# Kernel optimization log

Measured on AMD Instinct MI355X. Metric: run time of the kernel, lower is better.

Reference implementation:

```python
import jax, jax.numpy as jnp
import numpy as np

B, L, D = 1, 4096, 1024
N_AR, N_DIFF, D_HEAD = 8, 8, 64
H = N_AR + N_DIFF
ROPE_BASE = 10000.0


def rotate_half(x):
    x1, x2 = jnp.split(x, 2, axis=-1)
    return jnp.concatenate([-x2, x1], axis=-1)


def rope_cos_sin(seq_len, d_head):
    inv_freq = 1.0 / (ROPE_BASE ** (jnp.arange(0, d_head, 2, dtype=jnp.float32) / d_head))
    t = jnp.arange(seq_len, dtype=jnp.float32)
    freqs = t[:, None] * inv_freq[None, :]          # [L, d_head//2]
    emb = jnp.concatenate([freqs, freqs], axis=-1)  # [L, d_head]
    return jnp.cos(emb), jnp.sin(emb)


def setup_inputs() -> dict:
    key = jax.random.key(0)
    ks = jax.random.split(key, 5)
    return {
        "hidden_states": jax.random.normal(ks[0], (B, L, D), dtype=jnp.float32),
        "Wq": jax.random.normal(ks[1], (D, H * D_HEAD), dtype=jnp.float32) * 0.02,
        "Wk": jax.random.normal(ks[2], (D, H * D_HEAD), dtype=jnp.float32) * 0.02,
        "Wv": jax.random.normal(ks[3], (D, H * D_HEAD), dtype=jnp.float32) * 0.02,
        "Wo": jax.random.normal(ks[4], (H * D_HEAD, D), dtype=jnp.float32) * 0.02,
    }


def _attend(q, k, v, mask):
    # q,k,v: [B, h, L, d]; mask: [L, L] additive
    scale = D_HEAD ** -0.5
    scores = jnp.einsum("bhqd,bhkd->bhqk", q, k) * scale + mask
    attn = jax.nn.softmax(scores.astype(jnp.float32), axis=-1).astype(q.dtype)
    return jnp.einsum("bhqk,bhkd->bhqd", attn, v)


def reference(hidden_states, Wq, Wk, Wv, Wo):
    b, l, _ = hidden_states.shape

    def heads(x, W):
        return (x @ W).reshape(b, l, H, D_HEAD).transpose(0, 2, 1, 3)  # [B,H,L,d]

    q = heads(hidden_states, Wq)
    k = heads(hidden_states, Wk)
    v = heads(hidden_states, Wv)

    cos, sin = rope_cos_sin(l, D_HEAD)  # [L, d]
    q = q * cos + rotate_half(q) * sin
    k = k * cos + rotate_half(k) * sin

    neg_inf = jnp.finfo(jnp.float32).min
    causal = jnp.where(jnp.tril(jnp.ones((l, l), dtype=bool)), 0.0, -jnp.inf).astype(jnp.float32)

    out_ar = _attend(q[:, :N_AR], k[:, :N_AR], v[:, :N_AR], causal)
    out_diff = _attend(q[:, N_AR:], k[:, N_AR:], v[:, N_AR:], jnp.zeros((l, l), jnp.float32))

    out = jnp.concatenate([out_ar, out_diff], axis=1)          # [B,H,L,d]
    out = out.transpose(0, 2, 1, 3).reshape(b, l, H * D_HEAD)  # [B,L,H*d]
    return out @ Wo
```

## Files before the change

kernel.cpp:

```cpp
#include <hip/hip_runtime.h>

#define LSEQ 4096
#define DMODEL 1024
#define HTOT 16
#define NAR 8
#define DHEAD 64
#define QKVS 3072

typedef unsigned short u16;
typedef unsigned int u32;
typedef __attribute__((ext_vector_type(8))) short bf16x8;
typedef __attribute__((ext_vector_type(4))) short bf16x4;
typedef __attribute__((ext_vector_type(4))) float f32x4;
typedef __attribute__((ext_vector_type(4))) unsigned int u32x4;

typedef __attribute__((address_space(1))) void gvoid;
typedef __attribute__((address_space(3))) void lvoid;

__device__ __forceinline__ void cp16(const void* g, void* l) {
    __builtin_amdgcn_global_load_lds((gvoid*)(void*)g, (lvoid*)l, 16, 0, 0);
}

__device__ __forceinline__ u16 f2bf(float f) {
    u32 x = __float_as_uint(f);
    return (u16)((x + 0x7fffu + ((x >> 16) & 1u)) >> 16);
}
__device__ __forceinline__ u32 packtr(float lo, float hi) {
    return __builtin_amdgcn_perm(__float_as_uint(hi), __float_as_uint(lo), 0x07060302u);
}

__global__ __launch_bounds__(256) void xcast(const float* __restrict__ X, u16* __restrict__ Xb)
{
    const size_t i = (size_t)(blockIdx.x * 256 + threadIdx.x) * 8;
    float4 a0 = *(const float4*)(X + i);
    float4 a1 = *(const float4*)(X + i + 4);
    uint4 pk;
    pk.x = packtr(a0.x, a0.y); pk.y = packtr(a0.z, a0.w);
    pk.z = packtr(a1.x, a1.y); pk.w = packtr(a1.z, a1.w);
    *(uint4*)(Xb + i) = pk;
}

__global__ __launch_bounds__(256) void transp_cvt3(
    const float* __restrict__ Wq, const float* __restrict__ Wk,
    const float* __restrict__ Wv, u16* __restrict__ D)
{
    __shared__ u16 T[64][72];
    const float* S = (blockIdx.z == 0) ? Wq : ((blockIdx.z == 1) ? Wk : Wv);
    u16* Dz = D + (size_t)blockIdx.z * 1024 * 1024;
    const int tid = threadIdx.x;
    const int bx = blockIdx.x, by = blockIdx.y;
#pragma unroll
    for (int i = 0; i < 4; ++i) {
        int id = tid + i * 256;
        int fr = id >> 4, fc = id & 15;
        float4 v = *(const float4*)(S + (size_t)(by * 64 + fr) * 1024 + bx * 64 + fc * 4);
        T[fc * 4 + 0][fr] = f2bf(v.x);
        T[fc * 4 + 1][fr] = f2bf(v.y);
        T[fc * 4 + 2][fr] = f2bf(v.z);
        T[fc * 4 + 3][fr] = f2bf(v.w);
    }
    __syncthreads();
#pragma unroll
    for (int i = 0; i < 2; ++i) {
        int id = tid + i * 256;
        int c = id >> 3, g = id & 7;
        *(uint4*)(Dz + (size_t)(bx * 64 + c) * 1024 + by * 64 + g * 8) = *(const uint4*)&T[c][g * 8];
    }
}

__global__ __launch_bounds__(256) void transp_cvt(
    const float* __restrict__ S, u16* __restrict__ D)
{
    __shared__ u16 T[64][72];
    const int tid = threadIdx.x;
    const int bx = blockIdx.x, by = blockIdx.y;
#pragma unroll
    for (int i = 0; i < 4; ++i) {
        int id = tid + i * 256;
        int fr = id >> 4, fc = id & 15;
        float4 v = *(const float4*)(S + (size_t)(by * 64 + fr) * 1024 + bx * 64 + fc * 4);
        T[fc * 4 + 0][fr] = f2bf(v.x);
        T[fc * 4 + 1][fr] = f2bf(v.y);
        T[fc * 4 + 2][fr] = f2bf(v.z);
        T[fc * 4 + 3][fr] = f2bf(v.w);
    }
    __syncthreads();
#pragma unroll
    for (int i = 0; i < 2; ++i) {
        int id = tid + i * 256;
        int c = id >> 3, g = id & 7;
        *(uint4*)(D + (size_t)(bx * 64 + c) * 1024 + by * 64 + g * 8) = *(const uint4*)&T[c][g * 8];
    }
}

__global__ __launch_bounds__(256) void gemm_qkv(
    const u16* __restrict__ A, const u16* __restrict__ Bt, u16* __restrict__ C)
{
    __shared__ u16 As[2][128][32];
    __shared__ u16 Bs[2][128][32];
    const int tid = threadIdx.x;
    const int lane = tid & 63, w = tid >> 6;
    const int col = lane & 15, quad = lane >> 4;
    const int bm = blockIdx.y << 7, bn = blockIdx.x << 7;
    const int wm = (w & 1) << 6, wn = (w >> 1) << 6;
    const int sr = lane >> 2, sc = (lane & 3) << 3;
    const f32x4 zero = {0.f, 0.f, 0.f, 0.f};
    f32x4 acc[4][4];
#pragma unroll
    for (int i = 0; i < 4; ++i)
#pragma unroll
        for (int j = 0; j < 4; ++j) acc[i][j] = zero;

#pragma unroll
    for (int i = 0; i < 2; ++i) {
        const int r0 = w * 32 + i * 16;
        cp16(A  + (size_t)(bm + r0 + sr) * 1024 + sc, &As[0][r0][0]);
        cp16(Bt + (size_t)(bn + r0 + sr) * 1024 + sc, &Bs[0][r0][0]);
    }

    for (int kc = 0; kc < 32; ++kc) {
        const int cur = kc & 1, nxt = cur ^ 1;
        __syncthreads();
        if (kc + 1 < 32) {
            const int k1 = (kc + 1) * 32;
#pragma unroll
            for (int i = 0; i < 2; ++i) {
                const int r0 = w * 32 + i * 16;
                cp16(A  + (size_t)(bm + r0 + sr) * 1024 + k1 + sc, &As[nxt][r0][0]);
                cp16(Bt + (size_t)(bn + r0 + sr) * 1024 + k1 + sc, &Bs[nxt][r0][0]);
            }
        }
        bf16x8 af[4], bfr[4];
#pragma unroll
        for (int i = 0; i < 4; ++i) af[i] = *(const bf16x8*)&As[cur][wm + i * 16 + col][quad * 8];
#pragma unroll
        for (int j = 0; j < 4; ++j) bfr[j] = *(const bf16x8*)&Bs[cur][wn + j * 16 + col][quad * 8];
#pragma unroll
        for (int i = 0; i < 4; ++i)
#pragma unroll
            for (int j = 0; j < 4; ++j)
                acc[i][j] = __builtin_amdgcn_mfma_f32_16x16x32_bf16(af[i], bfr[j], acc[i][j], 0, 0, 0);
    }

    if (blockIdx.x < 16) {
        const float scale = (blockIdx.x < 8) ? 0.18033688011112042f : 1.0f;
        const float inv0 = __expf((float)col * -0.2878231366242557f);
        const float inv1 = __expf((float)(16 + col) * -0.2878231366242557f);
#pragma unroll
        for (int i = 0; i < 4; ++i)
#pragma unroll
            for (int r = 0; r < 4; ++r) {
                const float t = (float)(bm + wm + i * 16 + quad * 4 + r);
                float s0, c0, s1, c1;
                __sincosf(t * inv0, &s0, &c0);
                __sincosf(t * inv1, &s1, &c1);
                float a0 = acc[i][0][r], b0 = acc[i][2][r];
                acc[i][0][r] = (a0 * c0 - b0 * s0) * scale;
                acc[i][2][r] = (b0 * c0 + a0 * s0) * scale;
                float a1 = acc[i][1][r], b1 = acc[i][3][r];
                acc[i][1][r] = (a1 * c1 - b1 * s1) * scale;
                acc[i][3][r] = (b1 * c1 + a1 * s1) * scale;
            }
    }
#pragma unroll
    for (int i = 0; i < 4; ++i)
#pragma unroll
        for (int j = 0; j < 4; ++j)
#pragma unroll
            for (int r = 0; r < 4; ++r)
                C[(size_t)(bm + wm + i * 16 + quad * 4 + r) * QKVS + bn + wn + j * 16 + col] =
                    f2bf(acc[i][j][r]);
}

__global__ __launch_bounds__(256) void gemm_out(
    const u16* __restrict__ A, const u16* __restrict__ Bt, float* __restrict__ C)
{
    __shared__ u16 As[2][128][32];
    __shared__ u16 Bs[2][64][32];
    const int tid = threadIdx.x;
    const int lane = tid & 63, w = tid >> 6;
    const int col = lane & 15, quad = lane >> 4;
    const int bm = blockIdx.y << 7, bn = blockIdx.x << 6;
    const int wm = (w & 1) << 6, wn = (w >> 1) << 5;
    const int sr = lane >> 2, sc = (lane & 3) << 3;
    const f32x4 zero = {0.f, 0.f, 0.f, 0.f};
    f32x4 acc[4][2];
#pragma unroll
    for (int i = 0; i < 4; ++i)
#pragma unroll
        for (int j = 0; j < 2; ++j) acc[i][j] = zero;

    {
#pragma unroll
        for (int i = 0; i < 2; ++i) {
            const int r0 = w * 32 + i * 16;
            cp16(A + (size_t)(bm + r0 + sr) * 1024 + sc, &As[0][r0][0]);
        }
        cp16(Bt + (size_t)(bn + w * 16 + sr) * 1024 + sc, &Bs[0][w * 16][0]);
    }

    for (int kc = 0; kc < 32; ++kc) {
        const int cur = kc & 1, nxt = cur ^ 1;
        __syncthreads();
        if (kc + 1 < 32) {
            const int k1 = (kc + 1) * 32;
#pragma unroll
            for (int i = 0; i < 2; ++i) {
                const int r0 = w * 32 + i * 16;
                cp16(A + (size_t)(bm + r0 + sr) * 1024 + k1 + sc, &As[nxt][r0][0]);
            }
            cp16(Bt + (size_t)(bn + w * 16 + sr) * 1024 + k1 + sc, &Bs[nxt][w * 16][0]);
        }
        bf16x8 af[4], bfr[2];
#pragma unroll
        for (int i = 0; i < 4; ++i) af[i] = *(const bf16x8*)&As[cur][wm + i * 16 + col][quad * 8];
#pragma unroll
        for (int j = 0; j < 2; ++j) bfr[j] = *(const bf16x8*)&Bs[cur][wn + j * 16 + col][quad * 8];
#pragma unroll
        for (int i = 0; i < 4; ++i)
#pragma unroll
            for (int j = 0; j < 2; ++j)
                acc[i][j] = __builtin_amdgcn_mfma_f32_16x16x32_bf16(af[i], bfr[j], acc[i][j], 0, 0, 0);
    }
#pragma unroll
    for (int i = 0; i < 4; ++i)
#pragma unroll
        for (int j = 0; j < 2; ++j)
#pragma unroll
            for (int r = 0; r < 4; ++r)
                C[(size_t)(bm + wm + i * 16 + quad * 4 + r) * 1024 + bn + wn + j * 16 + col] =
                    acc[i][j][r];
}

__global__ __launch_bounds__(256) void attn_mfma(
    const u16* __restrict__ QKV, u16* __restrict__ AO)
{
    __shared__ u16 Ks[2][128][64];
    __shared__ u16 Vt[64][136];
    const int bid = blockIdx.x;
    int h, qt;
    if (bid < 256) { h = 8 + (bid & 7); qt = bid >> 3; }
    else { int i = bid - 256; h = i & 7; qt = 31 - (i >> 3); }
    const bool causal = (h < NAR);
    const int tid = threadIdx.x;
    const int w = tid >> 6, lane = tid & 63;
    const int col = lane & 15, quad = lane >> 4;
    const int qb = qt * 128;
    const int qr0 = qb + w * 32 + col;
    const int qr1 = qr0 + 16;
    const int cva = ((lane >> 1) & 3) * 32 + (lane >> 3) * 4 + (lane & 1) * 2;

    bf16x8 qf[2][2];
#pragma unroll
    for (int s = 0; s < 2; ++s)
#pragma unroll
        for (int ks = 0; ks < 2; ++ks)
            qf[s][ks] = *(const bf16x8*)(QKV + (size_t)(qr0 + s * 16) * QKVS +
                                         h * DHEAD + ks * 32 + quad * 8);

    bf16x8 ones8;
#pragma unroll
    for (int i = 0; i < 8; ++i) ones8[i] = (short)0x3F80;

    const f32x4 zero = {0.f, 0.f, 0.f, 0.f};
    f32x4 O[2][5];
#pragma unroll
    for (int s = 0; s < 2; ++s)
#pragma unroll
        for (int nd = 0; nd < 5; ++nd) O[s][nd] = zero;

    const int nch = causal ? (qt + 1) : (LSEQ / 128);
    const int krow = lane >> 3;
    const int kcb = (lane & 7) ^ krow;
    const u16* kbase = QKV + (size_t)krow * QKVS + 1024 + h * DHEAD + kcb * 8;
    const u16* vbase = QKV + (size_t)(lane * 2) * QKVS + 2048 + h * DHEAD + w * 16;

    u32x4 vA0, vA1, vB0, vB1;
    bf16x8 pf8[2][4];

#define VT_WRITE()                                                                                 \
    _Pragma("unroll")                                                                              \
    for (int j = 0; j < 4; ++j) {                                                                  \
        *(u32*)&Vt[w * 16 + 2 * j][cva]         = __builtin_amdgcn_perm(vB0[j], vA0[j], 0x05040100u); \
        *(u32*)&Vt[w * 16 + 2 * j + 1][cva]     = __builtin_amdgcn_perm(vB0[j], vA0[j], 0x07060302u); \
        *(u32*)&Vt[w * 16 + 8 + 2 * j][cva]     = __builtin_amdgcn_perm(vB1[j], vA1[j], 0x05040100u); \
        *(u32*)&Vt[w * 16 + 8 + 2 * j + 1][cva] = __builtin_amdgcn_perm(vB1[j], vA1[j], 0x07060302u); \
    }

#define PV_STEP()                                                                                  \
    {                                                                                              \
        __builtin_amdgcn_s_setprio(1);                                                             \
        _Pragma("unroll")                                                                          \
        for (int tp = 0; tp < 4; ++tp) {                                                           \
            bf16x8 vv[4];                                                                          \
            _Pragma("unroll")                                                                      \
            for (int nd = 0; nd < 4; ++nd)                                                         \
                vv[nd] = *(const bf16x8*)&Vt[nd * 16 + col][quad * 32 + tp * 8];                   \
            _Pragma("unroll")                                                                      \
            for (int nd = 0; nd < 4; ++nd) {                                                       \
                O[0][nd] = __builtin_amdgcn_mfma_f32_16x16x32_bf16(vv[nd], pf8[0][tp], O[0][nd], 0, 0, 0); \
                O[1][nd] = __builtin_amdgcn_mfma_f32_16x16x32_bf16(vv[nd], pf8[1][tp], O[1][nd], 0, 0, 0); \
            }                                                                                      \
            O[0][4] = __builtin_amdgcn_mfma_f32_16x16x32_bf16(ones8, pf8[0][tp], O[0][4], 0, 0, 0); \
            O[1][4] = __builtin_amdgcn_mfma_f32_16x16x32_bf16(ones8, pf8[1][tp], O[1][4], 0, 0, 0); \
        }                                                                                          \
        __builtin_amdgcn_s_setprio(0);                                                             \
    }

#define S_STEP(KBUF, CH)                                                                           \
    {                                                                                              \
        const bool mask = causal && ((CH) == qt);                                                  \
        _Pragma("unroll")                                                                          \
        for (int hf = 0; hf < 2; ++hf) {                                                           \
            f32x4 st[2][4];                                                                        \
            _Pragma("unroll")                                                                      \
            for (int s = 0; s < 2; ++s)                                                            \
                _Pragma("unroll")                                                                  \
                for (int jj = 0; jj < 4; ++jj) st[s][jj] = zero;                                   \
            __builtin_amdgcn_s_setprio(1);                                                         \
            _Pragma("unroll")                                                                      \
            for (int ks = 0; ks < 2; ++ks)                                                         \
                _Pragma("unroll")                                                                  \
                for (int jj = 0; jj < 4; ++jj) {                                                   \
                    bf16x8 kf = *(const bf16x8*)&Ks[KBUF][(hf * 4 + jj) * 16 + col]                \
                                                         [((ks * 4 + quad) ^ (col & 7)) * 8];      \
                    st[0][jj] = __builtin_amdgcn_mfma_f32_16x16x32_bf16(kf, qf[0][ks], st[0][jj], 0, 0, 0); \
                    st[1][jj] = __builtin_amdgcn_mfma_f32_16x16x32_bf16(kf, qf[1][ks], st[1][jj], 0, 0, 0); \
                }                                                                                  \
            __builtin_amdgcn_s_setprio(0);                                                         \
            if (mask) {                                                                            \
                _Pragma("unroll")                                                                  \
                for (int jj = 0; jj < 4; ++jj) {                                                   \
                    const int kk = (CH) * 128 + (hf * 4 + jj) * 16 + quad * 4;                     \
                    _Pragma("unroll")                                                              \
                    for (int r = 0; r < 4; ++r) {                                                  \
                        if (kk + r > qr0) st[0][jj][r] = -1e30f;                                   \
                        if (kk + r > qr1) st[1][jj][r] = -1e30f;                                   \
                    }                                                                              \
                }                                                                                  \
            }                                                                                      \
            _Pragma("unroll")                                                                      \
            for (int s = 0; s < 2; ++s)                                                            \
                _Pragma("unroll")                                                                  \
                for (int jj = 0; jj < 4; ++jj) {                                                   \
                    u32 plo = packtr(__builtin_amdgcn_exp2f(st[s][jj][0]),                         \
                                     __builtin_amdgcn_exp2f(st[s][jj][1]));                        \
                    u32 phi = packtr(__builtin_amdgcn_exp2f(st[s][jj][2]),                         \
                                     __builtin_amdgcn_exp2f(st[s][jj][3]));                        \
                    u32* p = (u32*)&pf8[s][0] + (hf * 4 + jj) * 2;                                 \
                    p[0] = plo; p[1] = phi;                                                        \
                }                                                                                  \
        }                                                                                          \
    }

#pragma unroll
    for (int i = 0; i < 4; ++i)
        cp16(kbase + (size_t)((i * 4 + w) * 8) * QKVS, &Ks[0][(i * 4 + w) * 8][0]);
    vA0 = *(u32x4*)(vbase);
    vA1 = *(u32x4*)(vbase + 8);
    vB0 = *(u32x4*)(vbase + QKVS);
    vB1 = *(u32x4*)(vbase + QKVS + 8);
    __syncthreads();
    VT_WRITE();
    if (nch > 1) {
#pragma unroll
        for (int i = 0; i < 4; ++i)
            cp16(kbase + (size_t)(128 + (i * 4 + w) * 8) * QKVS, &Ks[1][(i * 4 + w) * 8][0]);
    }
    S_STEP(0, 0);

    for (int ch = 1; ch < nch; ++ch) {
        const int cur = ch & 1;
        __syncthreads();
        if (ch + 1 < nch) {
            const size_t c1 = (size_t)(ch + 1) * 128;
#pragma unroll
            for (int i = 0; i < 4; ++i)
                cp16(kbase + (c1 + (i * 4 + w) * 8) * QKVS, &Ks[cur ^ 1][(i * 4 + w) * 8][0]);
        }
        {
            const u16* vp = vbase + (size_t)ch * 128 * QKVS;
            vA0 = *(u32x4*)(vp);
            vA1 = *(u32x4*)(vp + 8);
            vB0 = *(u32x4*)(vp + QKVS);
            vB1 = *(u32x4*)(vp + QKVS + 8);
        }
        PV_STEP();
        S_STEP(cur, ch);
        __syncthreads();
        VT_WRITE();
    }

    __syncthreads();
    PV_STEP();

#pragma unroll
    for (int s = 0; s < 2; ++s) {
        const float inv = 1.f / O[s][4][0];
        const int qrow = qr0 + s * 16;
#pragma unroll
        for (int nd = 0; nd < 4; ++nd) {
            ushort4 ov;
            ov.x = f2bf(O[s][nd][0] * inv);
            ov.y = f2bf(O[s][nd][1] * inv);
            ov.z = f2bf(O[s][nd][2] * inv);
            ov.w = f2bf(O[s][nd][3] * inv);
            *(ushort4*)(AO + (size_t)qrow * 1024 + h * DHEAD + nd * 16 + quad * 4) = ov;
        }
    }
#undef VT_WRITE
#undef PV_STEP
#undef S_STEP
}

extern "C" void kernel_launch(void* const* d_in, const int* in_sizes, int n_in,
                              void* d_out, int out_size, void* d_ws, size_t ws_size,
                              hipStream_t stream)
{
    const float* X  = (const float*)d_in[0];
    const float* Wq = (const float*)d_in[1];
    const float* Wk = (const float*)d_in[2];
    const float* Wv = (const float*)d_in[3];
    const float* Wo = (const float*)d_in[4];
    float* out = (float*)d_out;

    u16* Wt  = (u16*)d_ws;
    u16* AOb = (u16*)d_ws;
    u16* QKV = (u16*)d_ws + (size_t)4 * 1024 * 1024;
    u16* Wot = QKV;
    u16* Xb  = (u16*)out;

    xcast<<<2048, 256, 0, stream>>>(X, Xb);
    transp_cvt3<<<dim3(16, 16, 3), 256, 0, stream>>>(Wq, Wk, Wv, Wt);
    gemm_qkv<<<dim3(24, 32), 256, 0, stream>>>(Xb, Wt, QKV);
    attn_mfma<<<512, 256, 0, stream>>>(QKV, AOb);
    transp_cvt<<<dim3(16, 16), 256, 0, stream>>>(Wo, Wot);
    gemm_out<<<dim3(16, 32), 256, 0, stream>>>(AOb, Wot, out);
}
```

Measured before the change: 241.8 us.

## Split non-causal attention tiles across two blocks and merge partials

Most non-causal (diffusion) head tiles are split into two key-range halves computed by separate blocks. Each half writes unnormalized fp32 partial outputs and row sums to scratch in the output buffer, and a new merge kernel adds and normalizes them into the bf16 attention output. The grid grows to 768 slots so work is spread more evenly across CUs alongside the causal tiles. The cost is an extra kernel launch and scratch-memory traffic for the partials.

```diff
diff --git a/kernel.cpp b/kernel.cpp
--- a/kernel.cpp
+++ b/kernel.cpp
@@ -232,15 +232,63 @@
                     acc[i][j][r];
 }
 
+__global__ __launch_bounds__(256) void merge_attn(
+    const float* __restrict__ OS, u16* __restrict__ AO)
+{
+    const int jid = blockIdx.x;
+    const int h = 8 + (jid & 7), qt = jid >> 3;
+    const float* P0 = OS + (size_t)(2 * jid) * 8320;
+    const float* P1 = P0 + 8320;
+    const int tid = threadIdx.x;
+    const int q = tid >> 1, d0 = (tid & 1) * 32;
+    const float inv = 1.f / (P0[8192 + q] + P1[8192 + q]);
+    const float* a = P0 + q * 64 + d0;
+    const float* b = P1 + q * 64 + d0;
+    u16* dst = AO + (size_t)(qt * 128 + q) * 1024 + h * 64 + d0;
+#pragma unroll
+    for (int v = 0; v < 4; ++v) {
+        u32 pk[4];
+#pragma unroll
+        for (int m = 0; m < 4; ++m) {
+            const int e = v * 8 + m * 2;
+            float lo = (a[e] + b[e]) * inv;
+            float hi = (a[e + 1] + b[e + 1]) * inv;
+            pk[m] = ((u32)f2bf(lo)) | (((u32)f2bf(hi)) << 16);
+        }
+        uint4 o; o.x = pk[0]; o.y = pk[1]; o.z = pk[2]; o.w = pk[3];
+        *(uint4*)(dst + v * 8) = o;
+    }
+}
+
 __global__ __launch_bounds__(256) void attn_mfma(
-    const u16* __restrict__ QKV, u16* __restrict__ AO)
+    const u16* __restrict__ QKV, u16* __restrict__ AO, float* __restrict__ OS)
 {
     __shared__ u16 Ks[2][128][64];
     __shared__ u16 Vt[64][136];
     const int bid = blockIdx.x;
-    int h, qt;
-    if (bid < 256) { h = 8 + (bid & 7); qt = bid >> 3; }
-    else { int i = bid - 256; h = i & 7; qt = 31 - (i >> 3); }
+    const int t = bid & 255, slot = bid >> 8;
+    int h, qt, c0, c1;
+    int pidx = -1;
+    if (t < 128) {
+        if (slot == 0)      { h = t & 7; qt = t >> 3; }
+        else if (slot == 1) { h = t & 7; qt = 31 - (t >> 3); }
+        else                { pidx = t; }
+    } else if (t < 252) {
+        pidx = 128 + 3 * (t - 128) + slot;
+    } else {
+        if (slot == 0)      { h = 8 + (t & 7); qt = t >> 3; }
+        else if (slot == 1) { pidx = 500 + (t - 252); }
+        else return;
+    }
+    bool split = false;
+    if (pidx >= 0) {
+        split = true;
+        const int jid = pidx >> 1, p = pidx & 1;
+        h = 8 + (jid & 7); qt = jid >> 3;
+        c0 = p * 16; c1 = c0 + 16;
+    } else {
+        c0 = 0; c1 = (h < NAR) ? (qt + 1) : 32;
+    }
     const bool causal = (h < NAR);
     const int tid = threadIdx.x;
     const int w = tid >> 6, lane = tid & 63;
@@ -269,7 +317,6 @@
 #pragma unroll
         for (int nd = 0; nd < 5; ++nd) O[s][nd] = zero;
 
-    const int nch = causal ? (qt + 1) : (LSEQ / 128);
     const int krow = lane >> 3;
     const int kcb = (lane & 7) ^ krow;
     const u16* kbase = QKV + (size_t)krow * QKVS + 1024 + h * DHEAD + kcb * 8;
@@ -355,28 +402,31 @@
 
 #pragma unroll
     for (int i = 0; i < 4; ++i)
-        cp16(kbase + (size_t)((i * 4 + w) * 8) * QKVS, &Ks[0][(i * 4 + w) * 8][0]);
-    vA0 = *(u32x4*)(vbase);
-    vA1 = *(u32x4*)(vbase + 8);
-    vB0 = *(u32x4*)(vbase + QKVS);
-    vB1 = *(u32x4*)(vbase + QKVS + 8);
+        cp16(kbase + (size_t)(c0 * 128 + (i * 4 + w) * 8) * QKVS, &Ks[0][(i * 4 + w) * 8][0]);
+    {
+        const u16* vp = vbase + (size_t)c0 * 128 * QKVS;
+        vA0 = *(u32x4*)(vp);
+        vA1 = *(u32x4*)(vp + 8);
+        vB0 = *(u32x4*)(vp + QKVS);
+        vB1 = *(u32x4*)(vp + QKVS + 8);
+    }
     __syncthreads();
     VT_WRITE();
-    if (nch > 1) {
+    if (c1 - c0 > 1) {
 #pragma unroll
         for (int i = 0; i < 4; ++i)
-            cp16(kbase + (size_t)(128 + (i * 4 + w) * 8) * QKVS, &Ks[1][(i * 4 + w) * 8][0]);
-    }
-    S_STEP(0, 0);
-
-    for (int ch = 1; ch < nch; ++ch) {
-        const int cur = ch & 1;
+            cp16(kbase + (size_t)((c0 + 1) * 128 + (i * 4 + w) * 8) * QKVS, &Ks[1][(i * 4 + w) * 8][0]);
+    }
+    S_STEP(0, c0);
+
+    for (int ch = c0 + 1; ch < c1; ++ch) {
+        const int rel = (ch - c0) & 1;
         __syncthreads();
-        if (ch + 1 < nch) {
-            const size_t c1 = (size_t)(ch + 1) * 128;
+        if (ch + 1 < c1) {
+            const size_t cc = (size_t)(ch + 1) * 128;
 #pragma unroll
             for (int i = 0; i < 4; ++i)
-                cp16(kbase + (c1 + (i * 4 + w) * 8) * QKVS, &Ks[cur ^ 1][(i * 4 + w) * 8][0]);
+                cp16(kbase + (cc + (i * 4 + w) * 8) * QKVS, &Ks[rel ^ 1][(i * 4 + w) * 8][0]);
         }
         {
             const u16* vp = vbase + (size_t)ch * 128 * QKVS;
@@ -386,7 +436,7 @@
             vB1 = *(u32x4*)(vp + QKVS + 8);
         }
         PV_STEP();
-        S_STEP(cur, ch);
+        S_STEP(rel, ch);
         __syncthreads();
         VT_WRITE();
     }
@@ -394,18 +444,31 @@
     __syncthreads();
     PV_STEP();
 
-#pragma unroll
-    for (int s = 0; s < 2; ++s) {
-        const float inv = 1.f / O[s][4][0];
-        const int qrow = qr0 + s * 16;
-#pragma unroll
-        for (int nd = 0; nd < 4; ++nd) {
-            ushort4 ov;
-            ov.x = f2bf(O[s][nd][0] * inv);
-            ov.y = f2bf(O[s][nd][1] * inv);
-            ov.z = f2bf(O[s][nd][2] * inv);
-            ov.w = f2bf(O[s][nd][3] * inv);
-            *(ushort4*)(AO + (size_t)qrow * 1024 + h * DHEAD + nd * 16 + quad * 4) = ov;
+    if (!split) {
+#pragma unroll
+        for (int s = 0; s < 2; ++s) {
+            const float inv = 1.f / O[s][4][0];
+            const int qrow = qr0 + s * 16;
+#pragma unroll
+            for (int nd = 0; nd < 4; ++nd) {
+                ushort4 ov;
+                ov.x = f2bf(O[s][nd][0] * inv);
+                ov.y = f2bf(O[s][nd][1] * inv);
+                ov.z = f2bf(O[s][nd][2] * inv);
+                ov.w = f2bf(O[s][nd][3] * inv);
+                *(ushort4*)(AO + (size_t)qrow * 1024 + h * DHEAD + nd * 16 + quad * 4) = ov;
+            }
+        }
+    } else {
+        float* P = OS + (size_t)pidx * 8320;
+        const int ql = w * 32 + col;
+#pragma unroll
+        for (int s = 0; s < 2; ++s) {
+            const int q = ql + s * 16;
+#pragma unroll
+            for (int nd = 0; nd < 4; ++nd)
+                *(f32x4*)(P + q * 64 + nd * 16 + quad * 4) = O[s][nd];
+            if (quad == 0) P[8192 + q] = O[s][4][0];
         }
     }
 #undef VT_WRITE
@@ -429,11 +492,13 @@
     u16* QKV = (u16*)d_ws + (size_t)4 * 1024 * 1024;
     u16* Wot = QKV;
     u16* Xb  = (u16*)out;
+    float* OS = out;
 
     xcast<<<2048, 256, 0, stream>>>(X, Xb);
     transp_cvt3<<<dim3(16, 16, 3), 256, 0, stream>>>(Wq, Wk, Wv, Wt);
     gemm_qkv<<<dim3(24, 32), 256, 0, stream>>>(Xb, Wt, QKV);
-    attn_mfma<<<512, 256, 0, stream>>>(QKV, AOb);
+    attn_mfma<<<768, 256, 0, stream>>>(QKV, AOb, OS);
     transp_cvt<<<dim3(16, 16), 256, 0, stream>>>(Wo, Wot);
+    merge_attn<<<252, 256, 0, stream>>>(OS, AOb);
     gemm_out<<<dim3(16, 32), 256, 0, stream>>>(AOb, Wot, out);
 }
```

New measurement: 247.3 us. +2.3%, slower.

## Split attention KV range across two wave groups with 1024-thread blocks sharing K/V tiles

Applied to the files above, without the earlier changes.

The attention kernel now launches 256 blocks of 1024 threads. Each block handles two adjacent query tiles of one head, and the key/value range is split between two groups of 8 waves, whose partial outputs and softmax denominators are combined through LDS at the end. K/V tiles are staged once per KV group and shared by both query tiles, which cuts redundant loads and balances causal work by pairing tiles. In exchange, LDS use and per-block thread count go up, occupancy drops to one large block, extra barriers and a reduction step are added, and causal groups may sit idle on masked chunks.

```diff
diff --git a/kernel.cpp b/kernel.cpp
--- a/kernel.cpp
+++ b/kernel.cpp
@@ -232,23 +232,36 @@
                     acc[i][j][r];
 }
 
-__global__ __launch_bounds__(256) void attn_mfma(
+__global__ __launch_bounds__(1024) void attn_mfma(
     const u16* __restrict__ QKV, u16* __restrict__ AO)
 {
-    __shared__ u16 Ks[2][128][64];
-    __shared__ u16 Vt[64][136];
+    __shared__ u16 POOL[2][25088];
     const int bid = blockIdx.x;
-    int h, qt;
-    if (bid < 256) { h = 8 + (bid & 7); qt = bid >> 3; }
-    else { int i = bid - 256; h = i & 7; qt = 31 - (i >> 3); }
+    int h, pair;
+    if (bid < 128) { h = 8 + (bid & 7); pair = bid >> 3; }
+    else { const int j = bid - 128; h = j & 7; pair = j >> 3; }
     const bool causal = (h < NAR);
+    const int qt0 = pair * 2;
+    const int L = causal ? (pair + 1) : 16;
+
     const int tid = threadIdx.x;
     const int w = tid >> 6, lane = tid & 63;
+    const int wkv = w >> 3;
+    const int wq = (w >> 2) & 1;
+    const int wl = w & 3;
+    const int w8 = w & 7;
     const int col = lane & 15, quad = lane >> 4;
-    const int qb = qt * 128;
-    const int qr0 = qb + w * 32 + col;
+    const int qtw = qt0 + wq;
+    const int qr0 = qtw * 128 + wl * 32 + col;
     const int qr1 = qr0 + 16;
+    const int c0 = wkv * L, c1 = c0 + L;
     const int cva = ((lane >> 1) & 3) * 32 + (lane >> 3) * 4 + (lane & 1) * 2;
+
+    u16 (*Ks0)[64] = (u16(*)[64]) & POOL[wkv][0];
+    u16 (*Ks1)[64] = (u16(*)[64]) & POOL[wkv][8192];
+    u16 (*Vt)[136] = (u16(*)[136]) & POOL[wkv][16384];
+    float* LDSX = (float*)&POOL[0][0];
+    float* LDSL = LDSX + 256 * 65;
 
     bf16x8 qf[2][2];
 #pragma unroll
@@ -269,22 +282,33 @@
 #pragma unroll
         for (int nd = 0; nd < 5; ++nd) O[s][nd] = zero;
 
-    const int nch = causal ? (qt + 1) : (LSEQ / 128);
     const int krow = lane >> 3;
     const int kcb = (lane & 7) ^ krow;
     const u16* kbase = QKV + (size_t)krow * QKVS + 1024 + h * DHEAD + kcb * 8;
-    const u16* vbase = QKV + (size_t)(lane * 2) * QKVS + 2048 + h * DHEAD + w * 16;
-
-    u32x4 vA0, vA1, vB0, vB1;
+    const u16* vbase = QKV + (size_t)(lane * 2) * QKVS + 2048 + h * DHEAD + w8 * 8;
+
+    u32x4 vA, vB;
     bf16x8 pf8[2][4];
+
+#define KSTAGE(DST, CH)                                                                            \
+    _Pragma("unroll")                                                                              \
+    for (int i = 0; i < 2; ++i) {                                                                  \
+        const int rb = i * 8 + w8;                                                                 \
+        cp16(kbase + (size_t)((CH) * 128 + rb * 8) * QKVS, &DST[rb * 8][0]);                       \
+    }
+
+#define VLOAD(CH)                                                                                  \
+    {                                                                                              \
+        const u16* vp = vbase + (size_t)(CH) * 128 * QKVS;                                         \
+        vA = *(u32x4*)(vp);                                                                        \
+        vB = *(u32x4*)(vp + QKVS);                                                                 \
+    }
 
 #define VT_WRITE()                                                                                 \
     _Pragma("unroll")                                                                              \
     for (int j = 0; j < 4; ++j) {                                                                  \
-        *(u32*)&Vt[w * 16 + 2 * j][cva]         = __builtin_amdgcn_perm(vB0[j], vA0[j], 0x05040100u); \
-        *(u32*)&Vt[w * 16 + 2 * j + 1][cva]     = __builtin_amdgcn_perm(vB0[j], vA0[j], 0x07060302u); \
-        *(u32*)&Vt[w * 16 + 8 + 2 * j][cva]     = __builtin_amdgcn_perm(vB1[j], vA1[j], 0x05040100u); \
-        *(u32*)&Vt[w * 16 + 8 + 2 * j + 1][cva] = __builtin_amdgcn_perm(vB1[j], vA1[j], 0x07060302u); \
+        *(u32*)&Vt[w8 * 8 + 2 * j][cva]     = __builtin_amdgcn_perm(vB[j], vA[j], 0x05040100u);    \
+        *(u32*)&Vt[w8 * 8 + 2 * j + 1][cva] = __builtin_amdgcn_perm(vB[j], vA[j], 0x07060302u);    \
     }
 
 #define PV_STEP()                                                                                  \
@@ -307,9 +331,9 @@
         __builtin_amdgcn_s_setprio(0);                                                             \
     }
 
-#define S_STEP(KBUF, CH)                                                                           \
+#define S_STEP(KB, CH)                                                                             \
     {                                                                                              \
-        const bool mask = causal && ((CH) == qt);                                                  \
+        const bool mask = causal && ((CH) == qtw);                                                 \
         _Pragma("unroll")                                                                          \
         for (int hf = 0; hf < 2; ++hf) {                                                           \
             f32x4 st[2][4];                                                                        \
@@ -322,8 +346,8 @@
             for (int ks = 0; ks < 2; ++ks)                                                         \
                 _Pragma("unroll")                                                                  \
                 for (int jj = 0; jj < 4; ++jj) {                                                   \
-                    bf16x8 kf = *(const bf16x8*)&Ks[KBUF][(hf * 4 + jj) * 16 + col]                \
-                                                         [((ks * 4 + quad) ^ (col & 7)) * 8];      \
+                    bf16x8 kf = *(const bf16x8*)&KB[(hf * 4 + jj) * 16 + col]                      \
+                                                  [((ks * 4 + quad) ^ (col & 7)) * 8];             \
                     st[0][jj] = __builtin_amdgcn_mfma_f32_16x16x32_bf16(kf, qf[0][ks], st[0][jj], 0, 0, 0); \
                     st[1][jj] = __builtin_amdgcn_mfma_f32_16x16x32_bf16(kf, qf[1][ks], st[1][jj], 0, 0, 0); \
                 }                                                                                  \
@@ -353,61 +377,63 @@
         }                                                                                          \
     }
 
-#pragma unroll
-    for (int i = 0; i < 4; ++i)
-        cp16(kbase + (size_t)((i * 4 + w) * 8) * QKVS, &Ks[0][(i * 4 + w) * 8][0]);
-    vA0 = *(u32x4*)(vbase);
-    vA1 = *(u32x4*)(vbase + 8);
-    vB0 = *(u32x4*)(vbase + QKVS);
-    vB1 = *(u32x4*)(vbase + QKVS + 8);
+    KSTAGE(Ks0, c0);
+    VLOAD(c0);
     __syncthreads();
     VT_WRITE();
-    if (nch > 1) {
-#pragma unroll
-        for (int i = 0; i < 4; ++i)
-            cp16(kbase + (size_t)(128 + (i * 4 + w) * 8) * QKVS, &Ks[1][(i * 4 + w) * 8][0]);
-    }
-    S_STEP(0, 0);
-
-    for (int ch = 1; ch < nch; ++ch) {
-        const int cur = ch & 1;
+    if (L > 1) { KSTAGE(Ks1, c0 + 1); }
+    if (!causal || c0 <= qtw) { S_STEP(Ks0, c0); }
+
+    for (int it = 1; it < L; ++it) {
+        const int ch = c0 + it;
+        u16 (*KB)[64] = (it & 1) ? Ks1 : Ks0;
+        u16 (*KN)[64] = (it & 1) ? Ks0 : Ks1;
         __syncthreads();
-        if (ch + 1 < nch) {
-            const size_t c1 = (size_t)(ch + 1) * 128;
-#pragma unroll
-            for (int i = 0; i < 4; ++i)
-                cp16(kbase + (c1 + (i * 4 + w) * 8) * QKVS, &Ks[cur ^ 1][(i * 4 + w) * 8][0]);
-        }
-        {
-            const u16* vp = vbase + (size_t)ch * 128 * QKVS;
-            vA0 = *(u32x4*)(vp);
-            vA1 = *(u32x4*)(vp + 8);
-            vB0 = *(u32x4*)(vp + QKVS);
-            vB1 = *(u32x4*)(vp + QKVS + 8);
-        }
-        PV_STEP();
-        S_STEP(cur, ch);
+        if (it + 1 < L) { KSTAGE(KN, ch + 1); }
+        VLOAD(ch);
+        if (!causal || (ch - 1) <= qtw) { PV_STEP(); }
+        if (!causal || ch <= qtw) { S_STEP(KB, ch); }
         __syncthreads();
         VT_WRITE();
     }
 
     __syncthreads();
-    PV_STEP();
-
-#pragma unroll
-    for (int s = 0; s < 2; ++s) {
-        const float inv = 1.f / O[s][4][0];
-        const int qrow = qr0 + s * 16;
-#pragma unroll
-        for (int nd = 0; nd < 4; ++nd) {
-            ushort4 ov;
-            ov.x = f2bf(O[s][nd][0] * inv);
-            ov.y = f2bf(O[s][nd][1] * inv);
-            ov.z = f2bf(O[s][nd][2] * inv);
-            ov.w = f2bf(O[s][nd][3] * inv);
-            *(ushort4*)(AO + (size_t)qrow * 1024 + h * DHEAD + nd * 16 + quad * 4) = ov;
+    if (!causal || (c1 - 1) <= qtw) { PV_STEP(); }
+
+    __syncthreads();
+    const int ql = wq * 128 + wl * 32 + col;
+    if (wkv == 1) {
+#pragma unroll
+        for (int s = 0; s < 2; ++s) {
+            const int q = ql + s * 16;
+#pragma unroll
+            for (int nd = 0; nd < 4; ++nd)
+                *(f32x4*)&LDSX[(size_t)q * 65 + nd * 16 + quad * 4] = O[s][nd];
+            if (quad == 0) LDSL[q] = O[s][4][0];
         }
     }
+    __syncthreads();
+    if (wkv == 0) {
+#pragma unroll
+        for (int s = 0; s < 2; ++s) {
+            const int q = ql + s * 16;
+            const float l = O[s][4][0] + LDSL[q];
+            const float inv = 1.f / l;
+            const int qrow = qr0 + s * 16;
+#pragma unroll
+            for (int nd = 0; nd < 4; ++nd) {
+                f32x4 pv = *(const f32x4*)&LDSX[(size_t)q * 65 + nd * 16 + quad * 4];
+                ushort4 ov;
+                ov.x = f2bf((O[s][nd][0] + pv[0]) * inv);
+                ov.y = f2bf((O[s][nd][1] + pv[1]) * inv);
+                ov.z = f2bf((O[s][nd][2] + pv[2]) * inv);
+                ov.w = f2bf((O[s][nd][3] + pv[3]) * inv);
+                *(ushort4*)(AO + (size_t)qrow * 1024 + h * DHEAD + nd * 16 + quad * 4) = ov;
+            }
+        }
+    }
+#undef KSTAGE
+#undef VLOAD
 #undef VT_WRITE
 #undef PV_STEP
 #undef S_STEP
@@ -433,7 +459,7 @@
     xcast<<<2048, 256, 0, stream>>>(X, Xb);
     transp_cvt3<<<dim3(16, 16, 3), 256, 0, stream>>>(Wq, Wk, Wv, Wt);
     gemm_qkv<<<dim3(24, 32), 256, 0, stream>>>(Xb, Wt, QKV);
-    attn_mfma<<<512, 256, 0, stream>>>(QKV, AOb);
+    attn_mfma<<<256, 1024, 0, stream>>>(QKV, AOb);
     transp_cvt<<<dim3(16, 16), 256, 0, stream>>>(Wo, Wot);
     gemm_out<<<dim3(16, 32), 256, 0, stream>>>(AOb, Wot, out);
 }
```

Result: slower. 365.2 us (+51.1%).
